# Performance work log

Hardware: AMD Instinct MI355X
Metric: run time of the kernel (lower is better)

The kernel has to match this reference:

```python
import jax, jax.numpy as jnp
import numpy as np

B, S, D, H = 2, 2048, 512, 8
HD = D // H
DFF = 4 * D
EPS_LN = 1e-5
EPS_ATTN = 1e-8


def layernorm(x, w, b):
    mu = jnp.mean(x, axis=-1, keepdims=True)
    var = jnp.var(x, axis=-1, keepdims=True)
    return (x - mu) * jax.lax.rsqrt(var + EPS_LN) * w + b


def masked_attention(q_src, v_src, wq, bq, wk, bk, wv, bv, wo, bo, M):
    # q_src/v_src: (B,S,D); M: (B,S,S)
    Bs, Ss, _ = q_src.shape
    Q = (q_src @ wq + bq).reshape(Bs, Ss, H, HD)
    K = (q_src @ wk + bk).reshape(Bs, Ss, H, HD)
    V = (v_src @ wv + bv).reshape(Bs, Ss, H, HD)
    scale = HD ** -0.5
    scores = jnp.einsum('bqhd,bkhd->bhqk', Q, K) * scale
    Mh = M[:, None, :, :]                      # (B,1,S,S) broadcast over heads
    scores = scores * Mh
    A = jax.nn.softmax(scores, axis=-1)
    A = A * Mh                                 # re-mask post-softmax
    A = A / (jnp.sum(jnp.abs(A), axis=-1, keepdims=True) + EPS_ATTN)  # L1 renorm
    out = jnp.einsum('bhqk,bkhd->bqhd', A, V).reshape(Bs, Ss, D)
    return out @ wo + bo


def ffn(x, w1, b1, w2, b2):
    h = jax.nn.gelu(x @ w1 + b1, approximate=False)
    return x + (h @ w2 + b2)                   # FeedForward(num_layers=2) includes residual


def setup_inputs() -> dict:
    key = jax.random.key(0)
    ks = iter(jax.random.split(key, 64))
    nrm = lambda shape, s=0.02: jax.random.normal(next(ks), shape, jnp.float32) * s
    d = {
        'gene_emb': jax.random.normal(next(ks), (B, S, D), jnp.float32),
        'expr_emb': jax.random.normal(next(ks), (B, S, D), jnp.float32),
        'M': jax.random.uniform(next(ks), (B, S, S), jnp.float32),
    }
    # gene attention params (weights stored (in,out))
    for p in ['g_wq', 'g_wk', 'g_wv', 'g_wo']:
        d[p] = nrm((D, D))
    for p in ['g_bq', 'g_bk', 'g_bv', 'g_bo']:
        d[p] = jnp.zeros((D,), jnp.float32)
    # expr attention params (fused proj 2D->D)
    d['e_wf'] = nrm((2 * D, D)); d['e_bf'] = jnp.zeros((D,), jnp.float32)
    for p in ['e_wq', 'e_wk', 'e_wv', 'e_wo']:
        d[p] = nrm((D, D))
    for p in ['e_bq', 'e_bk', 'e_bv', 'e_bo']:
        d[p] = jnp.zeros((D,), jnp.float32)
    # layernorms
    for p in ['ln_g1_w', 'ln_g2_w', 'ln_e1_w', 'ln_e2_w']:
        d[p] = jnp.ones((D,), jnp.float32)
    for p in ['ln_g1_b', 'ln_g2_b', 'ln_e1_b', 'ln_e2_b']:
        d[p] = jnp.zeros((D,), jnp.float32)
    # FFNs
    d['fg_w1'] = nrm((D, DFF)); d['fg_b1'] = jnp.zeros((DFF,), jnp.float32)
    d['fg_w2'] = nrm((DFF, D)); d['fg_b2'] = jnp.zeros((D,), jnp.float32)
    d['fe_w1'] = nrm((D, DFF)); d['fe_b1'] = jnp.zeros((DFF,), jnp.float32)
    d['fe_w2'] = nrm((DFF, D)); d['fe_b2'] = jnp.zeros((D,), jnp.float32)
    return d


def reference(gene_emb, expr_emb, M,
              g_wq, g_bq, g_wk, g_bk, g_wv, g_bv, g_wo, g_bo,
              e_wf, e_bf, e_wq, e_bq, e_wk, e_bk, e_wv, e_bv, e_wo, e_bo,
              ln_g1_w, ln_g1_b, ln_g2_w, ln_g2_b,
              ln_e1_w, ln_e1_b, ln_e2_w, ln_e2_b,
              fg_w1, fg_b1, fg_w2, fg_b2,
              fe_w1, fe_b1, fe_w2, fe_b2):
    # ----- gene branch -----
    xg = layernorm(gene_emb, ln_g1_w, ln_g1_b)
    attn_g = masked_attention(xg, xg, g_wq, g_bq, g_wk, g_bk, g_wv, g_bv, g_wo, g_bo, M)
    x = gene_emb + attn_g
    x_ln = layernorm(x, ln_g2_w, ln_g2_b)
    out_gene = x + ffn(x_ln, fg_w1, fg_b1, fg_w2, fg_b2)
    # ----- expression branch -----
    y_n = layernorm(expr_emb, ln_e1_w, ln_e1_b)
    fused = jnp.concatenate([gene_emb, y_n], axis=-1) @ e_wf + e_bf
    attn_e = masked_attention(fused, y_n, e_wq, e_bq, e_wk, e_bk, e_wv, e_bv, e_wo, e_bo, M)
    y = expr_emb + attn_e
    y_ln = layernorm(y, ln_e2_w, ln_e2_b)
    out_expr = y + ffn(y_ln, fe_w1, fe_b1, fe_w2, fe_b2)
    return (out_gene, out_expr)
```

## Files before the change

### kernel.cpp

```cpp
#include <hip/hip_runtime.h>
#include <math.h>

#define S_LEN 2048
#define DMODEL 512
#define NROWS 4096
#define NHEAD 8
#define HDIM 64
#define LOG2E 1.4426950408889634f

typedef __attribute__((ext_vector_type(8))) __bf16 bf16x8;
typedef __attribute__((ext_vector_type(4))) float f32x4;

__device__ inline float bf2f(unsigned short h) {
    unsigned u = ((unsigned)h) << 16;
    return __builtin_bit_cast(float, u);
}
__device__ inline unsigned short f2bf(float f) {
    unsigned u = __builtin_bit_cast(unsigned, f);
    return (unsigned short)((u + 0x7fffu + ((u >> 16) & 1u)) >> 16);
}

__device__ inline void gl_lds16(const unsigned short* g, unsigned short* l) {
    __builtin_amdgcn_global_load_lds(
        (const __attribute__((address_space(1))) void*)g,
        (__attribute__((address_space(3))) void*)l, 16, 0, 0);
}

__global__ __launch_bounds__(256) void wcast_t(
    const float* __restrict__ W, unsigned short* __restrict__ Wt, int K, int Mo)
{
    __shared__ float t[32][33];
    const int bx = blockIdx.x * 32;
    const int by = blockIdx.y * 32;
    const int tx = threadIdx.x & 31, ty = threadIdx.x >> 5;
    #pragma unroll
    for (int r = 0; r < 4; ++r)
        t[ty + 8 * r][tx] = W[(size_t)(by + ty + 8 * r) * Mo + bx + tx];
    __syncthreads();
    #pragma unroll
    for (int r = 0; r < 4; ++r)
        Wt[(size_t)(bx + ty + 8 * r) * K + by + tx] = f2bf(t[tx][ty + 8 * r]);
}

__global__ __launch_bounds__(256) void wcast_sq8(
    const float* w0, const float* w1, const float* w2, const float* w3,
    const float* w4, const float* w5, const float* w6, const float* w7,
    unsigned short* __restrict__ dst)
{
    const float* srcs[8] = {w0, w1, w2, w3, w4, w5, w6, w7};
    const float* __restrict__ W = srcs[blockIdx.z];
    unsigned short* __restrict__ Wt = dst + (size_t)blockIdx.z * 512 * 512;
    __shared__ float t[32][33];
    const int bx = blockIdx.x * 32, by = blockIdx.y * 32;
    const int tx = threadIdx.x & 31, ty = threadIdx.x >> 5;
    #pragma unroll
    for (int r = 0; r < 4; ++r)
        t[ty + 8 * r][tx] = W[(size_t)(by + ty + 8 * r) * 512 + bx + tx];
    __syncthreads();
    #pragma unroll
    for (int r = 0; r < 4; ++r)
        Wt[(size_t)(bx + ty + 8 * r) * 512 + by + tx] = f2bf(t[tx][ty + 8 * r]);
}

__global__ __launch_bounds__(256) void wcast_t2(
    const float* wA, const float* wB, unsigned short* __restrict__ dst,
    int K, int Mo)
{
    const float* __restrict__ W = blockIdx.z ? wB : wA;
    unsigned short* __restrict__ Wt = dst + (size_t)blockIdx.z * K * Mo;
    __shared__ float t[32][33];
    const int bx = blockIdx.x * 32, by = blockIdx.y * 32;
    const int tx = threadIdx.x & 31, ty = threadIdx.x >> 5;
    #pragma unroll
    for (int r = 0; r < 4; ++r)
        t[ty + 8 * r][tx] = W[(size_t)(by + ty + 8 * r) * Mo + bx + tx];
    __syncthreads();
    #pragma unroll
    for (int r = 0; r < 4; ++r)
        Wt[(size_t)(bx + ty + 8 * r) * K + by + tx] = f2bf(t[tx][ty + 8 * r]);
}

__global__ __launch_bounds__(256) void pack_bias(
    const float* __restrict__ b1, const float* __restrict__ b2,
    const float* __restrict__ b3, float* __restrict__ dst, int n)
{
    int t = blockIdx.x * 256 + threadIdx.x;
    if (t >= n) return;
    float v = (t < 512) ? b1[t] : (t < 1024) ? b2[t - 512] : b3[t - 1024];
    dst[t] = v;
}

__global__ __launch_bounds__(256) void cast_strided(
    const float* __restrict__ in, unsigned short* __restrict__ out, int ostride)
{
    const int row = blockIdx.x, t = threadIdx.x;
    out[(size_t)row * ostride + t]       = f2bf(in[(size_t)row * DMODEL + t]);
    out[(size_t)row * ostride + t + 256] = f2bf(in[(size_t)row * DMODEL + t + 256]);
}

__global__ __launch_bounds__(256) void ln_kernel(
    const float* __restrict__ x, const float* __restrict__ w,
    const float* __restrict__ b, unsigned short* __restrict__ y, int ostride)
{
    __shared__ float red[8];
    const int row = blockIdx.x;
    const float* xr = x + (size_t)row * DMODEL;
    const int t = threadIdx.x;
    float v0 = xr[t];
    float v1 = xr[t + 256];
    float s  = v0 + v1;
    float sq = v0 * v0 + v1 * v1;
    #pragma unroll
    for (int o = 32; o > 0; o >>= 1) {
        s  += __shfl_down(s, o);
        sq += __shfl_down(sq, o);
    }
    int wid = t >> 6, lane = t & 63;
    if (lane == 0) { red[wid] = s; red[4 + wid] = sq; }
    __syncthreads();
    float mean = (red[0] + red[1] + red[2] + red[3]) * (1.0f / 512.0f);
    float msq  = (red[4] + red[5] + red[6] + red[7]) * (1.0f / 512.0f);
    float var  = msq - mean * mean;
    float rs   = rsqrtf(var + 1e-5f);
    y[(size_t)row * ostride + t]       = f2bf((v0 - mean) * rs * w[t] + b[t]);
    y[(size_t)row * ostride + t + 256] = f2bf((v1 - mean) * rs * w[t + 256] + b[t + 256]);
}

__global__ __launch_bounds__(256) void vtrans(
    const unsigned short* __restrict__ V, int ldv, unsigned short* __restrict__ Vt)
{
    __shared__ unsigned short t[64][72];
    const int s0 = blockIdx.x * 64, h = blockIdx.y, b = blockIdx.z;
    const int tid = threadIdx.x;
    {
        const int r = tid >> 2, c = (tid & 3) * 16;
        const unsigned short* src = V + (size_t)(b * S_LEN + s0 + r) * ldv + h * 64 + c;
        *(int4*)&t[r][c]     = *(const int4*)(src);
        *(int4*)&t[r][c + 8] = *(const int4*)(src + 8);
    }
    __syncthreads();
    {
        const int d = tid >> 2, s = (tid & 3) * 16;
        unsigned short* dst = Vt + ((size_t)((b * 8 + h) * 64 + d)) * S_LEN + s0 + s;
        unsigned short tmp[16];
        #pragma unroll
        for (int e = 0; e < 16; ++e) tmp[e] = t[s + e][d];
        *(int4*)dst       = *(int4*)&tmp[0];
        *(int4*)(dst + 8) = *(int4*)&tmp[8];
    }
}

__global__ __launch_bounds__(256) void gemm_mfma(
    const unsigned short* __restrict__ A, int lda,
    const unsigned short* __restrict__ Bt,
    const float* __restrict__ bias,
    const float* __restrict__ R1,
    const unsigned short* __restrict__ R2,
    float* __restrict__ Cf, unsigned short* __restrict__ Cb,
    int K, int Mo, int dogelu)
{
    __shared__ __align__(16) unsigned short As[2][128 * 32];
    __shared__ __align__(16) unsigned short Bs[2][128 * 32];
    const int tid = threadIdx.x;
    const int wave = tid >> 6, lane = tid & 63;
    const int wr = wave >> 1, wc = wave & 1;
    const int row0 = blockIdx.y * 128, col0 = blockIdx.x * 128;
    const int l15 = lane & 15, q = lane >> 4;

    f32x4 acc[4][4];
    const f32x4 zz = {0.f, 0.f, 0.f, 0.f};
    #pragma unroll
    for (int i = 0; i < 4; ++i)
        #pragma unroll
        for (int j = 0; j < 4; ++j) acc[i][j] = zz;

    const int nk = K >> 5;
    #pragma unroll
    for (int r = 0; r < 2; ++r) {
        int idx = r * 256 + tid;
        int row = idx >> 2, kc = idx & 3;
        gl_lds16(&A[(size_t)(row0 + row) * lda + kc * 8],
                 &As[0][(size_t)(r * 256 + wave * 64) * 8]);
        gl_lds16(&Bt[(size_t)(col0 + row) * K + kc * 8],
                 &Bs[0][(size_t)(r * 256 + wave * 64) * 8]);
    }
    __syncthreads();

    for (int t = 0; t < nk; ++t) {
        const int cur = t & 1;
        if (t + 1 < nk) {
            const int k0 = (t + 1) * 32;
            #pragma unroll
            for (int r = 0; r < 2; ++r) {
                int idx = r * 256 + tid;
                int row = idx >> 2, kc = idx & 3;
                gl_lds16(&A[(size_t)(row0 + row) * lda + k0 + kc * 8],
                         &As[cur ^ 1][(size_t)(r * 256 + wave * 64) * 8]);
                gl_lds16(&Bt[(size_t)(col0 + row) * K + k0 + kc * 8],
                         &Bs[cur ^ 1][(size_t)(r * 256 + wave * 64) * 8]);
            }
        }
        bf16x8 af[4], bfr[4];
        #pragma unroll
        for (int fi = 0; fi < 4; ++fi)
            af[fi] = *(const bf16x8*)&As[cur][(wr * 64 + fi * 16 + l15) * 32 + q * 8];
        #pragma unroll
        for (int fj = 0; fj < 4; ++fj)
            bfr[fj] = *(const bf16x8*)&Bs[cur][(wc * 64 + fj * 16 + l15) * 32 + q * 8];
        #pragma unroll
        for (int fi = 0; fi < 4; ++fi)
            #pragma unroll
            for (int fj = 0; fj < 4; ++fj)
                acc[fi][fj] = __builtin_amdgcn_mfma_f32_16x16x32_bf16(
                    af[fi], bfr[fj], acc[fi][fj], 0, 0, 0);
        __syncthreads();
    }

    #pragma unroll
    for (int fi = 0; fi < 4; ++fi) {
        #pragma unroll
        for (int reg = 0; reg < 4; ++reg) {
            int row = row0 + wr * 64 + fi * 16 + q * 4 + reg;
            #pragma unroll
            for (int fj = 0; fj < 4; ++fj) {
                int col = col0 + wc * 64 + fj * 16 + l15;
                float v = acc[fi][fj][reg] + bias[col];
                if (dogelu) v = 0.5f * v * (1.0f + erff(v * 0.70710678118654752f));
                size_t off = (size_t)row * Mo + col;
                if (R1) v += R1[off];
                if (R2) v += bf2f(R2[off]);
                if (Cb) Cb[off] = f2bf(v);
                else    Cf[off] = v;
            }
        }
    }
}

__global__ __launch_bounds__(256) void gemm_mfma64(
    const unsigned short* __restrict__ A, int lda,
    const unsigned short* __restrict__ Bt,
    const float* __restrict__ bias,
    const float* __restrict__ R1,
    const unsigned short* __restrict__ R2,
    float* __restrict__ Cf, unsigned short* __restrict__ Cb,
    int K, int Mo, int dogelu)
{
    __shared__ __align__(16) unsigned short As[2][64 * 64];
    __shared__ __align__(16) unsigned short Bs[2][64 * 64];
    const int tid = threadIdx.x;
    const int wave = tid >> 6, lane = tid & 63;
    const int row0 = blockIdx.y * 64, col0 = blockIdx.x * 64;
    const int l15 = lane & 15, q = lane >> 4;

    f32x4 acc[4];
    const f32x4 zz = {0.f, 0.f, 0.f, 0.f};
    #pragma unroll
    for (int j = 0; j < 4; ++j) acc[j] = zz;

    const int nk = K >> 6;
    #pragma unroll
    for (int r = 0; r < 2; ++r) {
        int idx = r * 256 + tid;
        int row = idx >> 3;
        int kc  = (idx & 7) ^ (row & 7);
        gl_lds16(&A[(size_t)(row0 + row) * lda + kc * 8],
                 &As[0][(size_t)(r * 256 + wave * 64) * 8]);
        gl_lds16(&Bt[(size_t)(col0 + row) * K + kc * 8],
                 &Bs[0][(size_t)(r * 256 + wave * 64) * 8]);
    }
    __syncthreads();

    for (int t = 0; t < nk; ++t) {
        const int cur = t & 1;
        if (t + 1 < nk) {
            const int k0 = (t + 1) * 64;
            #pragma unroll
            for (int r = 0; r < 2; ++r) {
                int idx = r * 256 + tid;
                int row = idx >> 3;
                int kc  = (idx & 7) ^ (row & 7);
                gl_lds16(&A[(size_t)(row0 + row) * lda + k0 + kc * 8],
                         &As[cur ^ 1][(size_t)(r * 256 + wave * 64) * 8]);
                gl_lds16(&Bt[(size_t)(col0 + row) * K + k0 + kc * 8],
                         &Bs[cur ^ 1][(size_t)(r * 256 + wave * 64) * 8]);
            }
        }
        #pragma unroll
        for (int ks = 0; ks < 2; ++ks) {
            const int cx = ((ks * 4 + q) ^ (l15 & 7)) * 8;
            bf16x8 af = *(const bf16x8*)&As[cur][(wave * 16 + l15) * 64 + cx];
            bf16x8 bfr[4];
            #pragma unroll
            for (int fj = 0; fj < 4; ++fj)
                bfr[fj] = *(const bf16x8*)&Bs[cur][(fj * 16 + l15) * 64 + cx];
            #pragma unroll
            for (int fj = 0; fj < 4; ++fj)
                acc[fj] = __builtin_amdgcn_mfma_f32_16x16x32_bf16(af, bfr[fj], acc[fj], 0, 0, 0);
        }
        __syncthreads();
    }

    #pragma unroll
    for (int reg = 0; reg < 4; ++reg) {
        int row = row0 + wave * 16 + q * 4 + reg;
        #pragma unroll
        for (int fj = 0; fj < 4; ++fj) {
            int col = col0 + fj * 16 + l15;
            float v = acc[fj][reg] + bias[col];
            if (dogelu) v = 0.5f * v * (1.0f + erff(v * 0.70710678118654752f));
            size_t off = (size_t)row * Mo + col;
            if (R1) v += R1[off];
            if (R2) v += bf2f(R2[off]);
            if (Cb) Cb[off] = f2bf(v);
            else    Cf[off] = v;
        }
    }
}

__global__ __launch_bounds__(256, 4) void attn_mfma_split(
    const unsigned short* __restrict__ Q, int ldq,
    const unsigned short* __restrict__ Kp, int ldk,
    const unsigned short* __restrict__ Vt,
    const float* __restrict__ M,
    unsigned short* __restrict__ Opart,
    float* __restrict__ stats)
{
    __shared__ __align__(16) unsigned short Ks[64 * 72];
    __shared__ __align__(16) unsigned short Vs[64 * 72];
    __shared__ __align__(16) unsigned short Ps_all[4][16 * 72];

    const int bh = blockIdx.y, b = bh >> 3, h = bh & 7;
    const int q0 = blockIdx.x * 64;
    const int p = blockIdx.z;
    const int tid = threadIdx.x, wave = tid >> 6, lane = tid & 63;
    const int l15 = lane & 15, quad = lane >> 4;
    const int iRow = q0 + wave * 16 + l15;
    const int kBeg = p * (S_LEN / 2), kEnd = kBeg + (S_LEN / 2);

    unsigned short* Ps = &Ps_all[wave][0];

    bf16x8 qf[2];
    {
        const unsigned short* qp = Q + (size_t)(b * S_LEN + iRow) * ldq + h * HDIM + quad * 8;
        #pragma unroll
        for (int ks = 0; ks < 2; ++ks) {
            union { bf16x8 v; unsigned short u[8]; } tq;
            tq.v = *(const bf16x8*)(qp + ks * 32);
            #pragma unroll
            for (int e = 0; e < 8; ++e)
                tq.u[e] = f2bf(bf2f(tq.u[e]) * (0.125f * LOG2E));
            qf[ks] = tq.v;
        }
    }

    const int srow = tid >> 3;
    const int scol = (tid & 7) * 8;
    const unsigned short* kg = Kp + ((size_t)b * S_LEN) * ldk + h * HDIM + scol;
    const unsigned short* vg = Vt + ((size_t)bh * 64 + srow) * S_LEN + scol;
    const float* mrow = M + ((size_t)b * S_LEN + iRow) * S_LEN + quad * 4;

    float rm = -INFINITY, rZ = 0.f, rZm = 0.f;
    f32x4 oacc[4];
    const f32x4 zz = {0.f, 0.f, 0.f, 0.f};
    #pragma unroll
    for (int dt = 0; dt < 4; ++dt) oacc[dt] = zz;

    int4 kv0 = *(const int4*)(kg + (size_t)(kBeg + srow) * ldk);
    int4 kv1 = *(const int4*)(kg + (size_t)(kBeg + srow + 32) * ldk);
    int4 vv0 = *(const int4*)(vg + kBeg);
    int4 vv1 = *(const int4*)(vg + 32 * S_LEN + kBeg);
    *(int4*)&Ks[srow * 72 + scol]        = kv0;
    *(int4*)&Ks[(srow + 32) * 72 + scol] = kv1;
    *(int4*)&Vs[srow * 72 + scol]        = vv0;
    *(int4*)&Vs[(srow + 32) * 72 + scol] = vv1;
    __syncthreads();

    for (int k0 = kBeg; k0 < kEnd; k0 += 64) {
        const bool more = (k0 + 64 < kEnd);
        if (more) {
            kv0 = *(const int4*)(kg + (size_t)(k0 + 64 + srow) * ldk);
            kv1 = *(const int4*)(kg + (size_t)(k0 + 64 + srow + 32) * ldk);
            vv0 = *(const int4*)(vg + k0 + 64);
            vv1 = *(const int4*)(vg + 32 * S_LEN + k0 + 64);
        }
        float4 m4[4];
        #pragma unroll
        for (int jt = 0; jt < 4; ++jt)
            m4[jt] = *(const float4*)(mrow + k0 + jt * 16);

        f32x4 sacc[4];
        #pragma unroll
        for (int jt = 0; jt < 4; ++jt) sacc[jt] = zz;
        __builtin_amdgcn_s_setprio(1);
        #pragma unroll
        for (int jt = 0; jt < 4; ++jt) {
            bf16x8 kf0 = *(const bf16x8*)&Ks[(jt * 16 + l15) * 72 + quad * 8];
            bf16x8 kf1 = *(const bf16x8*)&Ks[(jt * 16 + l15) * 72 + 32 + quad * 8];
            sacc[jt] = __builtin_amdgcn_mfma_f32_16x16x32_bf16(kf0, qf[0], sacc[jt], 0, 0, 0);
            sacc[jt] = __builtin_amdgcn_mfma_f32_16x16x32_bf16(kf1, qf[1], sacc[jt], 0, 0, 0);
        }
        __builtin_amdgcn_s_setprio(0);

        float mx = -INFINITY;
        #pragma unroll
        for (int jt = 0; jt < 4; ++jt) {
            float mm[4] = {m4[jt].x, m4[jt].y, m4[jt].z, m4[jt].w};
            #pragma unroll
            for (int r = 0; r < 4; ++r) {
                sacc[jt][r] = sacc[jt][r] * mm[r];
                mx = fmaxf(mx, sacc[jt][r]);
            }
        }
        mx = fmaxf(mx, __shfl_xor(mx, 16));
        mx = fmaxf(mx, __shfl_xor(mx, 32));
        if (!__all(mx <= rm + 8.0f)) {
            float mn = fmaxf(rm, mx);
            float al = __builtin_amdgcn_exp2f(rm - mn);
            rm = mn; rZ *= al; rZm *= al;
            #pragma unroll
            for (int dt = 0; dt < 4; ++dt)
                #pragma unroll
                for (int r = 0; r < 4; ++r) oacc[dt][r] *= al;
        }

        float z = 0.f, zm = 0.f;
        #pragma unroll
        for (int jt = 0; jt < 4; ++jt) {
            float mm[4] = {m4[jt].x, m4[jt].y, m4[jt].z, m4[jt].w};
            float pv[4];
            #pragma unroll
            for (int r = 0; r < 4; ++r) {
                float e = __builtin_amdgcn_exp2f(sacc[jt][r] - rm);
                float pm = e * mm[r];
                z += e; zm += pm; pv[r] = pm;
            }
            unsigned lo, hi;
            asm("v_cvt_pk_bf16_f32 %0, %1, %2" : "=v"(lo) : "v"(pv[0]), "v"(pv[1]));
            asm("v_cvt_pk_bf16_f32 %0, %1, %2" : "=v"(hi) : "v"(pv[2]), "v"(pv[3]));
            uint2 pk; pk.x = lo; pk.y = hi;
            *(uint2*)&Ps[l15 * 72 + jt * 16 + quad * 4] = pk;
        }
        z  += __shfl_xor(z, 16);  z  += __shfl_xor(z, 32);
        zm += __shfl_xor(zm, 16); zm += __shfl_xor(zm, 32);
        rZ += z; rZm += zm;

        bf16x8 pf0 = *(const bf16x8*)&Ps[l15 * 72 + quad * 8];
        bf16x8 pf1 = *(const bf16x8*)&Ps[l15 * 72 + 32 + quad * 8];
        __builtin_amdgcn_s_setprio(1);
        #pragma unroll
        for (int dt = 0; dt < 4; ++dt) {
            bf16x8 vf0 = *(const bf16x8*)&Vs[(dt * 16 + l15) * 72 + quad * 8];
            bf16x8 vf1 = *(const bf16x8*)&Vs[(dt * 16 + l15) * 72 + 32 + quad * 8];
            oacc[dt] = __builtin_amdgcn_mfma_f32_16x16x32_bf16(vf0, pf0, oacc[dt], 0, 0, 0);
            oacc[dt] = __builtin_amdgcn_mfma_f32_16x16x32_bf16(vf1, pf1, oacc[dt], 0, 0, 0);
        }
        __builtin_amdgcn_s_setprio(0);

        if (more) {
            __syncthreads();
            *(int4*)&Ks[srow * 72 + scol]        = kv0;
            *(int4*)&Ks[(srow + 32) * 72 + scol] = kv1;
            *(int4*)&Vs[srow * 72 + scol]        = vv0;
            *(int4*)&Vs[(srow + 32) * 72 + scol] = vv1;
            __syncthreads();
        }
    }

    unsigned short* op = Opart + (((size_t)(p * 16 + bh) * S_LEN + iRow) * 64);
    #pragma unroll
    for (int dt = 0; dt < 4; ++dt) {
        unsigned lo, hi;
        asm("v_cvt_pk_bf16_f32 %0, %1, %2" : "=v"(lo) : "v"(oacc[dt][0]), "v"(oacc[dt][1]));
        asm("v_cvt_pk_bf16_f32 %0, %1, %2" : "=v"(hi) : "v"(oacc[dt][2]), "v"(oacc[dt][3]));
        uint2 o2; o2.x = lo; o2.y = hi;
        *(uint2*)(op + dt * 16 + quad * 4) = o2;
    }
    if (quad == 0) {
        float4 st; st.x = rm; st.y = rZ; st.z = rZm; st.w = 0.f;
        *(float4*)&stats[(((size_t)p * 16 + bh) * S_LEN + iRow) * 4] = st;
    }
}

__global__ __launch_bounds__(256) void attn_combine(
    const unsigned short* __restrict__ Opart, const float* __restrict__ stats,
    unsigned short* __restrict__ O)
{
    const int bh = blockIdx.y, b = bh >> 3, h = bh & 7;
    const int q0 = blockIdx.x * 64;
    const int tid = threadIdx.x;
    const int i = tid >> 2, dq = (tid & 3) * 16;
    const int qg = q0 + i;

    float4 s0 = *(const float4*)&stats[(((size_t)0 * 16 + bh) * S_LEN + qg) * 4];
    float4 s1 = *(const float4*)&stats[(((size_t)1 * 16 + bh) * S_LEN + qg) * 4];
    float ms = fmaxf(s0.x, s1.x);
    float w0 = __builtin_amdgcn_exp2f(s0.x - ms), w1 = __builtin_amdgcn_exp2f(s1.x - ms);
    float Z  = w0 * s0.y + w1 * s1.y;
    float Zm = w0 * s0.z + w1 * s1.z;
    float inv = 1.0f / (Zm + 1e-8f * Z);
    w0 *= inv; w1 *= inv;

    const unsigned short* p0 = Opart + (((size_t)0 * 16 + bh) * S_LEN + qg) * 64 + dq;
    const unsigned short* p1 = Opart + (((size_t)1 * 16 + bh) * S_LEN + qg) * 64 + dq;
    union { int4 v; unsigned short u[8]; } a0, a1, r;
    unsigned short* dst = O + (size_t)(b * S_LEN + qg) * DMODEL + h * HDIM + dq;
    #pragma unroll
    for (int half = 0; half < 2; ++half) {
        a0.v = *(const int4*)(p0 + half * 8);
        a1.v = *(const int4*)(p1 + half * 8);
        #pragma unroll
        for (int e = 0; e < 8; ++e)
            r.u[e] = f2bf(w0 * bf2f(a0.u[e]) + w1 * bf2f(a1.u[e]));
        *(int4*)(dst + half * 8) = r.v;
    }
}

extern "C" void kernel_launch(void* const* d_in, const int* in_sizes, int n_in,
                              void* d_out, int out_size, void* d_ws, size_t ws_size,
                              hipStream_t stream)
{
    const float* gene_emb = (const float*)d_in[0];
    const float* expr_emb = (const float*)d_in[1];
    const float* M        = (const float*)d_in[2];
    const float* g_wq = (const float*)d_in[3];
    const float* g_wk = (const float*)d_in[4];
    const float* g_wv = (const float*)d_in[5];
    const float* g_wo = (const float*)d_in[6];
    const float* g_bq = (const float*)d_in[7];
    const float* g_bk = (const float*)d_in[8];
    const float* g_bv = (const float*)d_in[9];
    const float* g_bo = (const float*)d_in[10];
    const float* e_wf = (const float*)d_in[11];
    const float* e_bf = (const float*)d_in[12];
    const float* e_wq = (const float*)d_in[13];
    const float* e_wk = (const float*)d_in[14];
    const float* e_wv = (const float*)d_in[15];
    const float* e_wo = (const float*)d_in[16];
    const float* e_bq = (const float*)d_in[17];
    const float* e_bk = (const float*)d_in[18];
    const float* e_bv = (const float*)d_in[19];
    const float* e_bo = (const float*)d_in[20];
    const float* ln_g1_w = (const float*)d_in[21];
    const float* ln_g2_w = (const float*)d_in[22];
    const float* ln_e1_w = (const float*)d_in[23];
    const float* ln_e2_w = (const float*)d_in[24];
    const float* ln_g1_b = (const float*)d_in[25];
    const float* ln_g2_b = (const float*)d_in[26];
    const float* ln_e1_b = (const float*)d_in[27];
    const float* ln_e2_b = (const float*)d_in[28];
    const float* fg_w1 = (const float*)d_in[29];
    const float* fg_b1 = (const float*)d_in[30];
    const float* fg_w2 = (const float*)d_in[31];
    const float* fg_b2 = (const float*)d_in[32];
    const float* fe_w1 = (const float*)d_in[33];
    const float* fe_b1 = (const float*)d_in[34];
    const float* fe_w2 = (const float*)d_in[35];
    const float* fe_b2 = (const float*)d_in[36];

    float* out_gene = (float*)d_out;
    float* out_expr = out_gene + (size_t)NROWS * DMODEL;

    char* ws = (char*)d_ws;
    const size_t MB1 = 1024 * 1024;
    unsigned short* bufA16  = (unsigned short*)(ws + 0 * MB1);
    unsigned short* bufAt16 = (unsigned short*)(ws + 4 * MB1);
    unsigned short* bufQKV  = (unsigned short*)(ws + 8 * MB1);
    unsigned short* bufQKe  = (unsigned short*)(ws + 8 * MB1);
    unsigned short* bufV16  = (unsigned short*)(ws + 16 * MB1);
    unsigned short* bufVt   = (unsigned short*)(ws + 20 * MB1);
    unsigned short* bufCat  = (unsigned short*)(ws + 24 * MB1);
    unsigned short* bufOp   = (unsigned short*)(ws + 24 * MB1);
    float*          bufSt   = (float*)(ws + 32 * MB1);
    float*          bufX    = (float*)(ws + 33 * MB1);
    unsigned short* bufH16  = (unsigned short*)(ws + 8 * MB1);
    char* wp = ws + 41 * MB1;
    unsigned short* sq8    = (unsigned short*)wp;
    unsigned short* gwq_t  = sq8 + 0 * 512 * 512;
    unsigned short* gwk_t  = sq8 + 1 * 512 * 512;
    unsigned short* gwv_t  = sq8 + 2 * 512 * 512;
    unsigned short* gwo_t  = sq8 + 3 * 512 * 512;
    unsigned short* ewq_t  = sq8 + 4 * 512 * 512;
    unsigned short* ewk_t  = sq8 + 5 * 512 * 512;
    unsigned short* ewv_t  = sq8 + 6 * 512 * 512;
    unsigned short* ewo_t  = sq8 + 7 * 512 * 512;
    unsigned short* ewf_t  = sq8 + 8 * 512 * 512;
    unsigned short* ffn1   = ewf_t + 1024 * 512;
    unsigned short* fgw1_t = ffn1;
    unsigned short* few1_t = ffn1 + 512 * 2048;
    unsigned short* ffn2   = few1_t + 512 * 2048;
    unsigned short* fgw2_t = ffn2;
    unsigned short* few2_t = ffn2 + 2048 * 512;
    float* biasg = (float*)(few2_t + 2048 * 512);
    float* biase = biasg + 1536;

    dim3 blk(256);
    dim3 ln_grid(NROWS);
    dim3 g512s(8, 64);
    dim3 g1024(8, 32);
    dim3 g1536(12, 32);
    dim3 g2048(16, 32);
    dim3 attn_grid(S_LEN / 64, 16, 2);
    dim3 comb_grid(S_LEN / 64, 16);
    dim3 vt_grid(S_LEN / 64, NHEAD, 2);

    wcast_sq8<<<dim3(16, 16, 8), blk, 0, stream>>>(
        g_wq, g_wk, g_wv, g_wo, e_wq, e_wk, e_wv, e_wo, sq8);
    wcast_t<<<dim3(16, 32), blk, 0, stream>>>(e_wf, ewf_t, 1024, 512);
    wcast_t2<<<dim3(64, 16, 2), blk, 0, stream>>>(fg_w1, fe_w1, ffn1, 512, 2048);
    wcast_t2<<<dim3(16, 64, 2), blk, 0, stream>>>(fg_w2, fe_w2, ffn2, 2048, 512);
    pack_bias<<<dim3(6), blk, 0, stream>>>(g_bq, g_bk, g_bv, biasg, 1536);
    pack_bias<<<dim3(4), blk, 0, stream>>>(e_bq, e_bk, e_bk, biase, 1024);

    ln_kernel<<<ln_grid, blk, 0, stream>>>(gene_emb, ln_g1_w, ln_g1_b, bufA16, 512);
    gemm_mfma<<<g1536, blk, 0, stream>>>(bufA16, 512, gwq_t, biasg, nullptr, nullptr, nullptr, bufQKV, 512, 1536, 0);
    vtrans<<<vt_grid, blk, 0, stream>>>(bufQKV + 1024, 1536, bufVt);
    attn_mfma_split<<<attn_grid, blk, 0, stream>>>(bufQKV, 1536, bufQKV + 512, 1536, bufVt, M, bufOp, bufSt);
    attn_combine<<<comb_grid, blk, 0, stream>>>(bufOp, bufSt, bufAt16);
    gemm_mfma64<<<g512s, blk, 0, stream>>>(bufAt16, 512, gwo_t, g_bo, gene_emb, nullptr, bufX, nullptr, 512, 512, 0);
    ln_kernel<<<ln_grid, blk, 0, stream>>>(bufX, ln_g2_w, ln_g2_b, bufA16, 512);
    gemm_mfma<<<g2048, blk, 0, stream>>>(bufA16, 512, fgw1_t, fg_b1, nullptr, nullptr, nullptr, bufH16, 512, 2048, 1);
    gemm_mfma64<<<g512s, blk, 0, stream>>>(bufH16, 2048, fgw2_t, fg_b2, bufX, bufA16, out_gene, nullptr, 2048, 512, 0);

    cast_strided<<<ln_grid, blk, 0, stream>>>(gene_emb, bufCat, 1024);
    ln_kernel<<<ln_grid, blk, 0, stream>>>(expr_emb, ln_e1_w, ln_e1_b, bufCat + 512, 1024);
    gemm_mfma64<<<g512s, blk, 0, stream>>>(bufCat, 1024, ewf_t, e_bf, nullptr, nullptr, nullptr, bufA16, 1024, 512, 0);
    gemm_mfma<<<g1024, blk, 0, stream>>>(bufA16, 512, ewq_t, biase, nullptr, nullptr, nullptr, bufQKe, 512, 1024, 0);
    gemm_mfma64<<<g512s, blk, 0, stream>>>(bufCat + 512, 1024, ewv_t, e_bv, nullptr, nullptr, nullptr, bufV16, 512, 512, 0);
    vtrans<<<vt_grid, blk, 0, stream>>>(bufV16, 512, bufVt);
    attn_mfma_split<<<attn_grid, blk, 0, stream>>>(bufQKe, 1024, bufQKe + 512, 1024, bufVt, M, bufOp, bufSt);
    attn_combine<<<comb_grid, blk, 0, stream>>>(bufOp, bufSt, bufAt16);
    gemm_mfma64<<<g512s, blk, 0, stream>>>(bufAt16, 512, ewo_t, e_bo, expr_emb, nullptr, bufX, nullptr, 512, 512, 0);
    ln_kernel<<<ln_grid, blk, 0, stream>>>(bufX, ln_e2_w, ln_e2_b, bufA16, 512);
    gemm_mfma<<<g2048, blk, 0, stream>>>(bufA16, 512, few1_t, fe_b1, nullptr, nullptr, nullptr, bufH16, 512, 2048, 1);
    gemm_mfma64<<<g512s, blk, 0, stream>>>(bufH16, 2048, few2_t, fe_b2, bufX, bufA16, out_expr, nullptr, 2048, 512, 0);
}
```

Measured before the change: 522.1 us.

## Retile N=512 GEMMs to 128x64, fuse cast into LN, defer attention row-sum reductions

The 64x64 GEMM for 512-wide outputs becomes a 128x64 tile with a K-step of 32 and a 2x2 wave layout, so each wave computes 4x2 MFMA fragments. This raises register-level reuse of the A and B fragments and halves the number of blocks. The new LDS layout drops the XOR swizzle, which risks bank conflicts. Separately, the gene-embedding cast is fused into the expression layernorm kernel, and the attention softmax row-sum cross-lane shuffles move out of the key loop to a single reduction at the end.

```diff
diff --git a/kernel.cpp b/kernel.cpp
--- a/kernel.cpp
+++ b/kernel.cpp
@@ -88,14 +88,6 @@
     if (t >= n) return;
     float v = (t < 512) ? b1[t] : (t < 1024) ? b2[t - 512] : b3[t - 1024];
     dst[t] = v;
-}
-
-__global__ __launch_bounds__(256) void cast_strided(
-    const float* __restrict__ in, unsigned short* __restrict__ out, int ostride)
-{
-    const int row = blockIdx.x, t = threadIdx.x;
-    out[(size_t)row * ostride + t]       = f2bf(in[(size_t)row * DMODEL + t]);
-    out[(size_t)row * ostride + t + 256] = f2bf(in[(size_t)row * DMODEL + t + 256]);
 }
 
 __global__ __launch_bounds__(256) void ln_kernel(
@@ -124,6 +116,39 @@
     float rs   = rsqrtf(var + 1e-5f);
     y[(size_t)row * ostride + t]       = f2bf((v0 - mean) * rs * w[t] + b[t]);
     y[(size_t)row * ostride + t + 256] = f2bf((v1 - mean) * rs * w[t + 256] + b[t + 256]);
+}
+
+__global__ __launch_bounds__(256) void ln_cat_kernel(
+    const float* __restrict__ xg, const float* __restrict__ xe,
+    const float* __restrict__ w, const float* __restrict__ b,
+    unsigned short* __restrict__ y)
+{
+    __shared__ float red[8];
+    const int row = blockIdx.x;
+    const int t = threadIdx.x;
+    const float* gr = xg + (size_t)row * DMODEL;
+    const float* er = xe + (size_t)row * DMODEL;
+    float g0 = gr[t], g1 = gr[t + 256];
+    float v0 = er[t], v1 = er[t + 256];
+    float s  = v0 + v1;
+    float sq = v0 * v0 + v1 * v1;
+    #pragma unroll
+    for (int o = 32; o > 0; o >>= 1) {
+        s  += __shfl_down(s, o);
+        sq += __shfl_down(sq, o);
+    }
+    int wid = t >> 6, lane = t & 63;
+    if (lane == 0) { red[wid] = s; red[4 + wid] = sq; }
+    __syncthreads();
+    float mean = (red[0] + red[1] + red[2] + red[3]) * (1.0f / 512.0f);
+    float msq  = (red[4] + red[5] + red[6] + red[7]) * (1.0f / 512.0f);
+    float var  = msq - mean * mean;
+    float rs   = rsqrtf(var + 1e-5f);
+    unsigned short* yr = y + (size_t)row * 1024;
+    yr[t]             = f2bf(g0);
+    yr[t + 256]       = f2bf(g1);
+    yr[512 + t]       = f2bf((v0 - mean) * rs * w[t] + b[t]);
+    yr[512 + t + 256] = f2bf((v1 - mean) * rs * w[t + 256] + b[t + 256]);
 }
 
 __global__ __launch_bounds__(256) void vtrans(
@@ -236,7 +261,7 @@
     }
 }
 
-__global__ __launch_bounds__(256) void gemm_mfma64(
+__global__ __launch_bounds__(256) void gemm_rect(
     const unsigned short* __restrict__ A, int lda,
     const unsigned short* __restrict__ Bt,
     const float* __restrict__ bias,
@@ -245,74 +270,85 @@
     float* __restrict__ Cf, unsigned short* __restrict__ Cb,
     int K, int Mo, int dogelu)
 {
-    __shared__ __align__(16) unsigned short As[2][64 * 64];
-    __shared__ __align__(16) unsigned short Bs[2][64 * 64];
+    __shared__ __align__(16) unsigned short As[2][128 * 32];
+    __shared__ __align__(16) unsigned short Bs[2][64 * 32];
     const int tid = threadIdx.x;
     const int wave = tid >> 6, lane = tid & 63;
-    const int row0 = blockIdx.y * 64, col0 = blockIdx.x * 64;
+    const int wr = wave >> 1, wc = wave & 1;
+    const int row0 = blockIdx.y * 128, col0 = blockIdx.x * 64;
     const int l15 = lane & 15, q = lane >> 4;
 
-    f32x4 acc[4];
+    f32x4 acc[4][2];
     const f32x4 zz = {0.f, 0.f, 0.f, 0.f};
     #pragma unroll
-    for (int j = 0; j < 4; ++j) acc[j] = zz;
-
-    const int nk = K >> 6;
+    for (int i = 0; i < 4; ++i)
+        #pragma unroll
+        for (int j = 0; j < 2; ++j) acc[i][j] = zz;
+
+    const int nk = K >> 5;
     #pragma unroll
     for (int r = 0; r < 2; ++r) {
         int idx = r * 256 + tid;
-        int row = idx >> 3;
-        int kc  = (idx & 7) ^ (row & 7);
+        int row = idx >> 2, kc = idx & 3;
         gl_lds16(&A[(size_t)(row0 + row) * lda + kc * 8],
                  &As[0][(size_t)(r * 256 + wave * 64) * 8]);
+    }
+    {
+        int row = tid >> 2, kc = tid & 3;
         gl_lds16(&Bt[(size_t)(col0 + row) * K + kc * 8],
-                 &Bs[0][(size_t)(r * 256 + wave * 64) * 8]);
+                 &Bs[0][(size_t)(wave * 64) * 8]);
     }
     __syncthreads();
 
     for (int t = 0; t < nk; ++t) {
         const int cur = t & 1;
         if (t + 1 < nk) {
-            const int k0 = (t + 1) * 64;
+            const int k0 = (t + 1) * 32;
             #pragma unroll
             for (int r = 0; r < 2; ++r) {
                 int idx = r * 256 + tid;
-                int row = idx >> 3;
-                int kc  = (idx & 7) ^ (row & 7);
+                int row = idx >> 2, kc = idx & 3;
                 gl_lds16(&A[(size_t)(row0 + row) * lda + k0 + kc * 8],
                          &As[cur ^ 1][(size_t)(r * 256 + wave * 64) * 8]);
+            }
+            {
+                int row = tid >> 2, kc = tid & 3;
                 gl_lds16(&Bt[(size_t)(col0 + row) * K + k0 + kc * 8],
-                         &Bs[cur ^ 1][(size_t)(r * 256 + wave * 64) * 8]);
+                         &Bs[cur ^ 1][(size_t)(wave * 64) * 8]);
             }
         }
-        #pragma unroll
-        for (int ks = 0; ks < 2; ++ks) {
-            const int cx = ((ks * 4 + q) ^ (l15 & 7)) * 8;
-            bf16x8 af = *(const bf16x8*)&As[cur][(wave * 16 + l15) * 64 + cx];
-            bf16x8 bfr[4];
-            #pragma unroll
-            for (int fj = 0; fj < 4; ++fj)
-                bfr[fj] = *(const bf16x8*)&Bs[cur][(fj * 16 + l15) * 64 + cx];
-            #pragma unroll
-            for (int fj = 0; fj < 4; ++fj)
-                acc[fj] = __builtin_amdgcn_mfma_f32_16x16x32_bf16(af, bfr[fj], acc[fj], 0, 0, 0);
-        }
+        bf16x8 af[4], bfr[2];
+        #pragma unroll
+        for (int fi = 0; fi < 4; ++fi)
+            af[fi] = *(const bf16x8*)&As[cur][(wr * 64 + fi * 16 + l15) * 32 + q * 8];
+        #pragma unroll
+        for (int fj = 0; fj < 2; ++fj)
+            bfr[fj] = *(const bf16x8*)&Bs[cur][(wc * 32 + fj * 16 + l15) * 32 + q * 8];
+        #pragma unroll
+        for (int fi = 0; fi < 4; ++fi)
+            #pragma unroll
+            for (int fj = 0; fj < 2; ++fj)
+                acc[fi][fj] = __builtin_amdgcn_mfma_f32_16x16x32_bf16(
+                    af[fi], bfr[fj], acc[fi][fj], 0, 0, 0);
         __syncthreads();
     }
 
     #pragma unroll
-    for (int reg = 0; reg < 4; ++reg) {
-        int row = row0 + wave * 16 + q * 4 + reg;
-        #pragma unroll
-        for (int fj = 0; fj < 4; ++fj) {
-            int col = col0 + fj * 16 + l15;
-            float v = acc[fj][reg] + bias[col];
-            if (dogelu) v = 0.5f * v * (1.0f + erff(v * 0.70710678118654752f));
-            size_t off = (size_t)row * Mo + col;
-            if (R1) v += R1[off];
-            if (R2) v += bf2f(R2[off]);
-            if (Cb) Cb[off] = f2bf(v);
-            else    Cf[off] = v;
+    for (int fi = 0; fi < 4; ++fi) {
+        #pragma unroll
+        for (int reg = 0; reg < 4; ++reg) {
+            int row = row0 + wr * 64 + fi * 16 + q * 4 + reg;
+            #pragma unroll
+            for (int fj = 0; fj < 2; ++fj) {
+                int col = col0 + wc * 32 + fj * 16 + l15;
+                float v = acc[fi][fj][reg] + bias[col];
+                if (dogelu) v = 0.5f * v * (1.0f + erff(v * 0.70710678118654752f));
+                size_t off = (size_t)row * Mo + col;
+                if (R1) v += R1[off];
+                if (R2) v += bf2f(R2[off]);
+                if (Cb) Cb[off] = f2bf(v);
+                else    Cf[off] = v;
+            }
         }
     }
 }
@@ -401,16 +437,17 @@
         }
         __builtin_amdgcn_s_setprio(0);
 
-        float mx = -INFINITY;
+        float mxj[4];
         #pragma unroll
         for (int jt = 0; jt < 4; ++jt) {
             float mm[4] = {m4[jt].x, m4[jt].y, m4[jt].z, m4[jt].w};
             #pragma unroll
-            for (int r = 0; r < 4; ++r) {
+            for (int r = 0; r < 4; ++r)
                 sacc[jt][r] = sacc[jt][r] * mm[r];
-                mx = fmaxf(mx, sacc[jt][r]);
-            }
-        }
+            mxj[jt] = fmaxf(fmaxf(sacc[jt][0], sacc[jt][1]),
+                            fmaxf(sacc[jt][2], sacc[jt][3]));
+        }
+        float mx = fmaxf(fmaxf(mxj[0], mxj[1]), fmaxf(mxj[2], mxj[3]));
         mx = fmaxf(mx, __shfl_xor(mx, 16));
         mx = fmaxf(mx, __shfl_xor(mx, 32));
         if (!__all(mx <= rm + 8.0f)) {
@@ -440,8 +477,6 @@
             uint2 pk; pk.x = lo; pk.y = hi;
             *(uint2*)&Ps[l15 * 72 + jt * 16 + quad * 4] = pk;
         }
-        z  += __shfl_xor(z, 16);  z  += __shfl_xor(z, 32);
-        zm += __shfl_xor(zm, 16); zm += __shfl_xor(zm, 32);
         rZ += z; rZm += zm;
 
         bf16x8 pf0 = *(const bf16x8*)&Ps[l15 * 72 + quad * 8];
@@ -465,6 +500,9 @@
             __syncthreads();
         }
     }
+
+    rZ  += __shfl_xor(rZ, 16);  rZ  += __shfl_xor(rZ, 32);
+    rZm += __shfl_xor(rZm, 16); rZm += __shfl_xor(rZm, 32);
 
     unsigned short* op = Opart + (((size_t)(p * 16 + bh) * S_LEN + iRow) * 64);
     #pragma unroll
@@ -595,7 +633,7 @@
 
     dim3 blk(256);
     dim3 ln_grid(NROWS);
-    dim3 g512s(8, 64);
+    dim3 gR512(8, 32);
     dim3 g1024(8, 32);
     dim3 g1536(12, 32);
     dim3 g2048(16, 32);
@@ -616,21 +654,20 @@
     vtrans<<<vt_grid, blk, 0, stream>>>(bufQKV + 1024, 1536, bufVt);
     attn_mfma_split<<<attn_grid, blk, 0, stream>>>(bufQKV, 1536, bufQKV + 512, 1536, bufVt, M, bufOp, bufSt);
     attn_combine<<<comb_grid, blk, 0, stream>>>(bufOp, bufSt, bufAt16);
-    gemm_mfma64<<<g512s, blk, 0, stream>>>(bufAt16, 512, gwo_t, g_bo, gene_emb, nullptr, bufX, nullptr, 512, 512, 0);
+    gemm_rect<<<gR512, blk, 0, stream>>>(bufAt16, 512, gwo_t, g_bo, gene_emb, nullptr, bufX, nullptr, 512, 512, 0);
     ln_kernel<<<ln_grid, blk, 0, stream>>>(bufX, ln_g2_w, ln_g2_b, bufA16, 512);
     gemm_mfma<<<g2048, blk, 0, stream>>>(bufA16, 512, fgw1_t, fg_b1, nullptr, nullptr, nullptr, bufH16, 512, 2048, 1);
-    gemm_mfma64<<<g512s, blk, 0, stream>>>(bufH16, 2048, fgw2_t, fg_b2, bufX, bufA16, out_gene, nullptr, 2048, 512, 0);
-
-    cast_strided<<<ln_grid, blk, 0, stream>>>(gene_emb, bufCat, 1024);
-    ln_kernel<<<ln_grid, blk, 0, stream>>>(expr_emb, ln_e1_w, ln_e1_b, bufCat + 512, 1024);
-    gemm_mfma64<<<g512s, blk, 0, stream>>>(bufCat, 1024, ewf_t, e_bf, nullptr, nullptr, nullptr, bufA16, 1024, 512, 0);
+    gemm_rect<<<gR512, blk, 0, stream>>>(bufH16, 2048, fgw2_t, fg_b2, bufX, bufA16, out_gene, nullptr, 2048, 512, 0);
+
+    ln_cat_kernel<<<ln_grid, blk, 0, stream>>>(gene_emb, expr_emb, ln_e1_w, ln_e1_b, bufCat);
+    gemm_rect<<<gR512, blk, 0, stream>>>(bufCat, 1024, ewf_t, e_bf, nullptr, nullptr, nullptr, bufA16, 1024, 512, 0);
     gemm_mfma<<<g1024, blk, 0, stream>>>(bufA16, 512, ewq_t, biase, nullptr, nullptr, nullptr, bufQKe, 512, 1024, 0);
-    gemm_mfma64<<<g512s, blk, 0, stream>>>(bufCat + 512, 1024, ewv_t, e_bv, nullptr, nullptr, nullptr, bufV16, 512, 512, 0);
+    gemm_rect<<<gR512, blk, 0, stream>>>(bufCat + 512, 1024, ewv_t, e_bv, nullptr, nullptr, nullptr, bufV16, 512, 512, 0);
     vtrans<<<vt_grid, blk, 0, stream>>>(bufV16, 512, bufVt);
     attn_mfma_split<<<attn_grid, blk, 0, stream>>>(bufQKe, 1024, bufQKe + 512, 1024, bufVt, M, bufOp, bufSt);
     attn_combine<<<comb_grid, blk, 0, stream>>>(bufOp, bufSt, bufAt16);
-    gemm_mfma64<<<g512s, blk, 0, stream>>>(bufAt16, 512, ewo_t, e_bo, expr_emb, nullptr, bufX, nullptr, 512, 512, 0);
+    gemm_rect<<<gR512, blk, 0, stream>>>(bufAt16, 512, ewo_t, e_bo, expr_emb, nullptr, bufX, nullptr, 512, 512, 0);
     ln_kernel<<<ln_grid, blk, 0, stream>>>(bufX, ln_e2_w, ln_e2_b, bufA16, 512);
     gemm_mfma<<<g2048, blk, 0, stream>>>(bufA16, 512, few1_t, fe_b1, nullptr, nullptr, nullptr, bufH16, 512, 2048, 1);
-    gemm_mfma64<<<g512s, blk, 0, stream>>>(bufH16, 2048, few2_t, fe_b2, bufX, bufA16, out_expr, nullptr, 2048, 512, 0);
-}
+    gemm_rect<<<gR512, blk, 0, stream>>>(bufH16, 2048, few2_t, fe_b2, bufX, bufA16, out_expr, nullptr, 2048, 512, 0);
+}
```

Measured after the change: 563.9 us. +8.0%, slower.
